# Optimization experiments

Hardware: AMD Instinct MI355X
Metric: run time of the kernel (lower is better)

The kernel has to match this reference:

```python
import jax, jax.numpy as jnp
import numpy as np
import math

B, D, L, H, K, CONV_N = 32, 128, 1024, 8, 7, 4
DK = D // H
EPS = 1e-5


def make_pos_encoding():
    i = np.arange(D, dtype=np.float64)
    freqs = np.where(i % 2 == 0, 10000.0 ** (-i / D), -(10000.0 ** ((1 - i) / D)))
    phases = np.where(i % 2 == 0, 0.0, math.pi / 2)
    pos = np.arange(L, dtype=np.float64)[None, :]  # [1, L]
    pe = np.sin(pos * freqs[:, None] + phases[:, None])  # [D, L]
    return jnp.asarray(pe, dtype=jnp.float32)


def layer_norm_2d(x, w, b):
    # nn.LayerNorm([D, L]) on [B, D, L]: normalize jointly over last two dims
    mu = jnp.mean(x, axis=(1, 2), keepdims=True)
    var = jnp.var(x, axis=(1, 2), keepdims=True)
    return (x - mu) * jax.lax.rsqrt(var + EPS) * w[None] + b[None]


def setup_inputs():
    key = jax.random.key(0)
    ks = jax.random.split(key, 24)
    s = 0.05
    x = jax.random.normal(ks[0], (B, D, L), jnp.float32)
    lengths = jax.random.randint(ks[1], (B,), L // 2, L + 1)
    mask = (jnp.arange(L)[None, :] >= lengths[:, None]).astype(jnp.float32)  # 1 = pad
    inp = {
        "x": x,
        "mask": mask,
        "pos_enc": make_pos_encoding(),
        "normb_w": jnp.ones((D, L), jnp.float32),
        "normb_b": jnp.zeros((D, L), jnp.float32),
        "dw_w": jax.random.normal(ks[2], (CONV_N, D, K), jnp.float32) * s,
        "dw_b": jnp.zeros((CONV_N, D), jnp.float32),
        "pw_w": jax.random.normal(ks[3], (CONV_N, D, D), jnp.float32) * s,
        "pw_b": jnp.zeros((CONV_N, D), jnp.float32),
        "norms_w": jnp.ones((CONV_N, D, L), jnp.float32),
        "norms_b": jnp.zeros((CONV_N, D, L), jnp.float32),
        "qw": jax.random.normal(ks[4], (D, D), jnp.float32) * s,
        "qb": jnp.zeros((D,), jnp.float32),
        "kw": jax.random.normal(ks[5], (D, D), jnp.float32) * s,
        "kb": jnp.zeros((D,), jnp.float32),
        "vw": jax.random.normal(ks[6], (D, D), jnp.float32) * s,
        "vb": jnp.zeros((D,), jnp.float32),
        "aw": jax.random.normal(ks[7], (D, D), jnp.float32) * s,  # attention output fc
        "ab": jnp.zeros((D,), jnp.float32),
        "norme_w": jnp.ones((D, L), jnp.float32),
        "norme_b": jnp.zeros((D, L), jnp.float32),
        "fw": jax.random.normal(ks[8], (D, D), jnp.float32) * s,  # final fc
        "fb": jnp.zeros((D,), jnp.float32),
    }
    return inp


def reference(x, mask, pos_enc, normb_w, normb_b, dw_w, dw_b, pw_w, pw_b,
              norms_w, norms_b, qw, qb, kw, kb, vw, vb, aw, ab,
              norme_w, norme_b, fw, fb):
    # positional encoding + pre-LN
    out = x + pos_enc[None]
    res = out
    out = layer_norm_2d(out, normb_w, normb_b)

    # conv stack (eval mode: dropout is identity)
    for i in range(CONV_N):
        h = jax.lax.conv_general_dilated(
            out, dw_w[i][:, None, :],  # depthwise: [D, 1, K]
            window_strides=(1,), padding=[(K // 2, K // 2)],
            dimension_numbers=("NCH", "OIH", "NCH"),
            feature_group_count=D) + dw_b[i][None, :, None]
        h = jnp.einsum("bcl,oc->bol", h, pw_w[i]) + pw_b[i][None, :, None]
        out = jax.nn.relu(h) + res
        res = out
        out = layer_norm_2d(out, norms_w[i], norms_b[i])

    # multi-head self-attention (manual bmm-softmax-bmm, scale 1/sqrt(d_k))
    xt = jnp.swapaxes(out, 1, 2)  # [B, L, D]
    q = (xt @ qw.T + qb).reshape(B, L, H, DK)
    k = (xt @ kw.T + kb).reshape(B, L, H, DK)
    v = (xt @ vw.T + vb).reshape(B, L, H, DK)
    scores = jnp.einsum("bqhd,bkhd->bhqk", q, k) * (1.0 / math.sqrt(DK))
    m = mask[:, None, None, :]  # broadcast over heads and query dim
    scores = scores * (1.0 - m) + m * (-1e30)
    attn = jax.nn.softmax(scores, axis=-1)
    o = jnp.einsum("bhqk,bkhd->bqhd", attn, v).reshape(B, L, D)
    o = o @ aw.T + ab
    o = jnp.swapaxes(o, 1, 2)  # [B, D, L]

    out = o + res
    res = out
    out = layer_norm_2d(out, norme_w, norme_b)
    out = jnp.einsum("bdl,ed->bel", out, fw) + fb[None, :, None]
    out = jax.nn.relu(out) + res
    return out
```

## Files before the change

### kernel.cpp

```cpp
#include <hip/hip_runtime.h>

#define NB 32
#define ND 128
#define NL 1024
#define NDL (ND*NL)
#define STATS_B 16
#define STATS_R (32*STATS_B)

typedef __attribute__((ext_vector_type(8))) short bf16x8;
typedef __attribute__((ext_vector_type(4))) float f32x4;
typedef unsigned short u16;

__device__ __forceinline__ f32x4 mfma_bf16_16x16x32(bf16x8 a, bf16x8 b, f32x4 c) {
#if defined(__HIP_DEVICE_COMPILE__)
  return __builtin_amdgcn_mfma_f32_16x16x32_bf16(a, b, c, 0, 0, 0);
#else
  return c;
#endif
}

__device__ __forceinline__ float exp2fast(float x) {
#if defined(__HIP_DEVICE_COMPILE__) && __has_builtin(__builtin_amdgcn_exp2f)
  return __builtin_amdgcn_exp2f(x);
#elif defined(__HIP_DEVICE_COMPILE__)
  return __expf(x * 0.6931471805599453f);
#else
  return x;
#endif
}

__device__ __forceinline__ float bf2f(u16 u) {
  union { unsigned u; float f; } c; c.u = ((unsigned)u) << 16; return c.f;
}
__device__ __forceinline__ u16 bf16rnd(float f) {
  union { float f; unsigned u; } c; c.f = f;
  return (u16)((c.u + 0x7FFFu + ((c.u >> 16) & 1u)) >> 16);
}
__device__ __forceinline__ unsigned packpair(float a, float b) {
  return (unsigned)bf16rnd(a) | ((unsigned)bf16rnd(b) << 16);
}
__device__ __forceinline__ unsigned packtrunc(float a, float b) {
  unsigned ua = __float_as_uint(a), ub = __float_as_uint(b);
  return (ub & 0xFFFF0000u) | (ua >> 16);
}
__device__ __forceinline__ bf16x8 packbf8(float4 a, float4 b) {
  union { unsigned u[4]; bf16x8 v; } r;
  r.u[0] = packpair(a.x, a.y); r.u[1] = packpair(a.z, a.w);
  r.u[2] = packpair(b.x, b.y); r.u[3] = packpair(b.z, b.w);
  return r.v;
}

__device__ __forceinline__ void blockRedAtomic(float s, float sq, float* base) {
  __shared__ float red[32];
#pragma unroll
  for (int off = 32; off > 0; off >>= 1) {
    s  += __shfl_down(s, off, 64);
    sq += __shfl_down(sq, off, 64);
  }
  int wave = threadIdx.x >> 6;
  int nw = blockDim.x >> 6;
  if ((threadIdx.x & 63) == 0) { red[wave*2] = s; red[wave*2+1] = sq; }
  __syncthreads();
  if (threadIdx.x == 0) {
    float ts = 0.f, tq = 0.f;
    for (int i = 0; i < nw; ++i) { ts += red[i*2]; tq += red[i*2+1]; }
    unsafeAtomicAdd(base,     ts);
    unsafeAtomicAdd(base + 1, tq);
  }
}

__global__ void k_zero(float* stats) {
  int t = threadIdx.x;
#pragma unroll
  for (int i = 0; i < 3; ++i) stats[i*1024 + t] = 0.f;
}

__global__ __launch_bounds__(256) void k_addpos(const float* __restrict__ x,
                                                const float* __restrict__ pe,
                                                u16* __restrict__ res,
                                                float* __restrict__ stats0) {
  int b = blockIdx.x >> 6;
  int off = ((blockIdx.x & 63) << 11) + (threadIdx.x << 3);
  const float4* xp = (const float4*)(x + (size_t)b*NDL + off);
  const float4* pp = (const float4*)(pe + off);
  float s = 0.f, sq = 0.f;
  float rv[8];
#pragma unroll
  for (int i = 0; i < 2; ++i) {
    float4 a = xp[i], p = pp[i];
    rv[i*4+0] = a.x + p.x; rv[i*4+1] = a.y + p.y;
    rv[i*4+2] = a.z + p.z; rv[i*4+3] = a.w + p.w;
  }
#pragma unroll
  for (int j = 0; j < 8; ++j) { s += rv[j]; sq += rv[j]*rv[j]; }
  uint4 pk;
  pk.x = packpair(rv[0], rv[1]); pk.y = packpair(rv[2], rv[3]);
  pk.z = packpair(rv[4], rv[5]); pk.w = packpair(rv[6], rv[7]);
  *(uint4*)(res + (size_t)b*NDL + off) = pk;
  blockRedAtomic(s, sq, stats0 + b*STATS_B);
}


__device__ __forceinline__ void load_w_frags16(const float* __restrict__ W,
                                               int wo, int lo, int hi, bf16x8 af[4]) {
#pragma unroll
  for (int kk = 0; kk < 4; ++kk) {
    const float4* wp = (const float4*)(W + (size_t)(wo + lo)*128 + kk*32 + hi*8);
    af[kk] = packbf8(wp[0], wp[1]);
  }
}

__device__ __forceinline__ void mfma_core16(const unsigned* xs, bf16x8 af[4],
                                            int lo, int hi, f32x4 acc[4]) {
#pragma unroll
  for (int ln = 0; ln < 4; ++ln) {
#pragma unroll
    for (int kk = 0; kk < 4; ++kk) {
      int l = ln*16 + lo;
      int off = (l*256 + kk*64 + hi*16) ^ ((lo & 7) << 4);
      bf16x8 bf = *(const bf16x8*)((const char*)xs + off);
      acc[ln] = mfma_bf16_16x16x32(af[kk], bf, acc[ln]);
    }
  }
}

__device__ __forceinline__ void conv_row8(const u16* __restrict__ srow,
                                          const float* __restrict__ lwrow,
                                          const float* __restrict__ lbrow,
                                          int base, float mu, float rstd,
                                          const float* wk, float bias0,
                                          float* h ) {
  float wa[14];
  bool interior = (base >= 4) && (base + 12 <= NL);
  if (interior) {
    const uint2* sp = (const uint2*)(srow + base - 4);
    const float4* wp = (const float4*)(lwrow + base - 4);
    const float4* bp = (const float4*)(lbrow + base - 4);
#pragma unroll
    for (int qd = 0; qd < 4; ++qd) {
      uint2 sv2 = sp[qd];
      float4 w4 = wp[qd], b4 = bp[qd];
      float sv[4] = {bf2f((u16)(sv2.x & 0xFFFF)), bf2f((u16)(sv2.x >> 16)),
                     bf2f((u16)(sv2.y & 0xFFFF)), bf2f((u16)(sv2.y >> 16))};
      float wv[4] = {w4.x, w4.y, w4.z, w4.w};
      float bv[4] = {b4.x, b4.y, b4.z, b4.w};
#pragma unroll
      for (int e = 0; e < 4; ++e) {
        int j = qd*4 + e - 1;
        if (j >= 0 && j < 14)
          wa[j] = (sv[e] - mu)*rstd*wv[e] + bv[e];
      }
    }
  } else {
#pragma unroll
    for (int j = 0; j < 14; ++j) {
      int gl = base + j - 3;
      float v = 0.f;
      if (gl >= 0 && gl < NL)
        v = (bf2f(srow[gl]) - mu)*rstd*lwrow[gl] + lbrow[gl];
      wa[j] = v;
    }
  }
#pragma unroll
  for (int l = 0; l < 8; ++l) {
    float acc = bias0;
#pragma unroll
    for (int j = 0; j < 7; ++j) acc += wa[l+j]*wk[j];
    h[l] = acc;
  }
}

template<int MODE>
__global__ __launch_bounds__(512) void k_gemm_mfma(
    const u16* __restrict__ src16, const float* __restrict__ W,
    const float* __restrict__ bias,
    const u16* __restrict__ res16, u16* __restrict__ wr16,
    float* __restrict__ outf,
    const float* __restrict__ lnw, const float* __restrict__ lnb,
    const float* __restrict__ dww, const float* __restrict__ dwb,
    const float* __restrict__ statsIn, float* __restrict__ statsOut) {
  __shared__ unsigned xs[4096];
  int b  = blockIdx.x >> 4;
  int l0 = (blockIdx.x & 15) << 6;
  int tid = threadIdx.x;
  int wave = tid >> 6, lane = tid & 63;
  int lo = lane & 15, hi = lane >> 4;
  int wo = wave * 16;

  float mu = 0.f, rstd = 0.f;
  if (MODE == 0 || MODE == 3) {
    mu = statsIn[b*STATS_B] * (1.f/NDL);
    rstd = rsqrtf(statsIn[b*STATS_B + 1]*(1.f/NDL) - mu*mu + 1e-5f);
  }

  if (MODE == 0) {
    int c2 = tid >> 3, lq = tid & 7;
    int c = c2*2, base = l0 + lq*8;
    float wk0[7], wk1[7];
#pragma unroll
    for (int j = 0; j < 7; ++j) { wk0[j] = dww[c*7 + j]; wk1[j] = dww[(c+1)*7 + j]; }
    const u16* sa = src16 + (size_t)b*NDL + (size_t)c*NL;
    const float* la  = lnw + (size_t)c*NL;
    const float* lbv = lnb + (size_t)c*NL;
    float h0[8], h1[8];
    conv_row8(sa,      la,      lbv,      base, mu, rstd, wk0, dwb[c],   h0);
    conv_row8(sa + NL, la + NL, lbv + NL, base, mu, rstd, wk1, dwb[c+1], h1);
#pragma unroll
    for (int l = 0; l < 8; ++l) {
      int ll = lq*8 + l;
      xs[(ll << 6) | (c2 ^ ((ll & 7) << 2))] = packpair(h0[l], h1[l]);
    }
  } else if (MODE == 1) {
    for (int i = tid; i < 1024; i += 512) {
      int c2 = i >> 4, lq = (i & 15) << 2;
      int c = c2*2;
      const u16* sp = src16 + (size_t)b*NDL + (size_t)c*NL + l0 + lq;
      uint2 ra = *(const uint2*)sp;
      uint2 rb = *(const uint2*)(sp + NL);
      unsigned wv[4];
      wv[0] = (ra.x & 0xFFFFu) | (rb.x << 16);
      wv[1] = (ra.x >> 16)     | (rb.x & 0xFFFF0000u);
      wv[2] = (ra.y & 0xFFFFu) | (rb.y << 16);
      wv[3] = (ra.y >> 16)     | (rb.y & 0xFFFF0000u);
#pragma unroll
      for (int j = 0; j < 4; ++j) {
        int l = lq + j;
        xs[(l << 6) | (c2 ^ ((l & 7) << 2))] = wv[j];
      }
    }
  } else {
    for (int i = tid; i < 1024; i += 512) {
      int c2 = i >> 4, lq = (i & 15) << 2;
      int c = c2*2;
      const u16* sp = src16 + (size_t)b*NDL + (size_t)c*NL + l0 + lq;
      uint2 ra = *(const uint2*)sp;
      uint2 rb = *(const uint2*)(sp + NL);
      float sa[4] = {bf2f((u16)(ra.x & 0xFFFF)), bf2f((u16)(ra.x >> 16)),
                     bf2f((u16)(ra.y & 0xFFFF)), bf2f((u16)(ra.y >> 16))};
      float sb[4] = {bf2f((u16)(rb.x & 0xFFFF)), bf2f((u16)(rb.x >> 16)),
                     bf2f((u16)(rb.y & 0xFFFF)), bf2f((u16)(rb.y >> 16))};
      size_t gi = (size_t)c*NL + l0 + lq;
      float4 w0 = *(const float4*)(lnw + gi), w1 = *(const float4*)(lnw + gi + NL);
      float4 bb0 = *(const float4*)(lnb + gi), bb1 = *(const float4*)(lnb + gi + NL);
      float va[4] = {(sa[0]-mu)*rstd*w0.x + bb0.x, (sa[1]-mu)*rstd*w0.y + bb0.y,
                     (sa[2]-mu)*rstd*w0.z + bb0.z, (sa[3]-mu)*rstd*w0.w + bb0.w};
      float vb[4] = {(sb[0]-mu)*rstd*w1.x + bb1.x, (sb[1]-mu)*rstd*w1.y + bb1.y,
                     (sb[2]-mu)*rstd*w1.z + bb1.z, (sb[3]-mu)*rstd*w1.w + bb1.w};
#pragma unroll
      for (int j = 0; j < 4; ++j) {
        int l = lq + j;
        xs[(l << 6) | (c2 ^ ((l & 7) << 2))] = packpair(va[j], vb[j]);
      }
    }
  }

  bf16x8 af[4];
  load_w_frags16(W, wo, lo, hi, af);
  f32x4 acc[4];
#pragma unroll
  for (int ln = 0; ln < 4; ++ln) acc[ln] = (f32x4){0.f,0.f,0.f,0.f};

  __syncthreads();
  mfma_core16(xs, af, lo, hi, acc);

  if (MODE == 0 || MODE == 1) {
    float s = 0.f, sq = 0.f;
#pragma unroll
    for (int ln = 0; ln < 4; ++ln) {
      int l = l0 + ln*16 + lo;
#pragma unroll
      for (int r = 0; r < 4; ++r) {
        int o = wo + hi*4 + r;
        size_t gi = ((size_t)b*ND + o)*NL + l;
        float v = acc[ln][r] + bias[o];
        if (MODE == 0) v = fmaxf(v, 0.f);
        v += bf2f(res16[gi]);
        wr16[gi] = bf16rnd(v);
        s += v; sq += v*v;
      }
    }
    blockRedAtomic(s, sq, statsOut + b*STATS_B);
  } else {
#pragma unroll
    for (int ln = 0; ln < 4; ++ln) {
      int l = l0 + ln*16 + lo;
#pragma unroll
      for (int r = 0; r < 4; ++r) {
        int o = wo + hi*4 + r;
        size_t gi = ((size_t)b*ND + o)*NL + l;
        outf[gi] = fmaxf(acc[ln][r] + bias[o], 0.f) + bf2f(res16[gi]);
      }
    }
  }
}

__global__ __launch_bounds__(512) void k_qkv_mfma(
    const u16* __restrict__ src16,
    const float* __restrict__ qw, const float* __restrict__ kw, const float* __restrict__ vw,
    const float* __restrict__ qb, const float* __restrict__ kb, const float* __restrict__ vb,
    u16* __restrict__ qo, u16* __restrict__ ko, u16* __restrict__ vo,
    const float* __restrict__ lnw, const float* __restrict__ lnb,
    const float* __restrict__ statsIn) {
  __shared__ unsigned xs[4096];
  int b  = blockIdx.x >> 4;
  int l0 = (blockIdx.x & 15) << 6;
  int tid = threadIdx.x;
  int wave = tid >> 6, lane = tid & 63;
  int lo = lane & 15, hi = lane >> 4;
  int wo = wave * 16;

  float mu = statsIn[b*STATS_B] * (1.f/NDL);
  float rstd = rsqrtf(statsIn[b*STATS_B + 1]*(1.f/NDL) - mu*mu + 1e-5f);
  for (int i = tid; i < 1024; i += 512) {
    int c2 = i >> 4, lq = (i & 15) << 2;
    int c = c2*2;
    const u16* sp = src16 + (size_t)b*NDL + (size_t)c*NL + l0 + lq;
    uint2 ra = *(const uint2*)sp;
    uint2 rb = *(const uint2*)(sp + NL);
    float sa[4] = {bf2f((u16)(ra.x & 0xFFFF)), bf2f((u16)(ra.x >> 16)),
                   bf2f((u16)(ra.y & 0xFFFF)), bf2f((u16)(ra.y >> 16))};
    float sb[4] = {bf2f((u16)(rb.x & 0xFFFF)), bf2f((u16)(rb.x >> 16)),
                   bf2f((u16)(rb.y & 0xFFFF)), bf2f((u16)(rb.y >> 16))};
    size_t gi = (size_t)c*NL + l0 + lq;
    float4 w0 = *(const float4*)(lnw + gi), w1 = *(const float4*)(lnw + gi + NL);
    float4 bb0 = *(const float4*)(lnb + gi), bb1 = *(const float4*)(lnb + gi + NL);
    float va[4] = {(sa[0]-mu)*rstd*w0.x + bb0.x, (sa[1]-mu)*rstd*w0.y + bb0.y,
                   (sa[2]-mu)*rstd*w0.z + bb0.z, (sa[3]-mu)*rstd*w0.w + bb0.w};
    float vb4[4] = {(sb[0]-mu)*rstd*w1.x + bb1.x, (sb[1]-mu)*rstd*w1.y + bb1.y,
                    (sb[2]-mu)*rstd*w1.z + bb1.z, (sb[3]-mu)*rstd*w1.w + bb1.w};
#pragma unroll
    for (int j = 0; j < 4; ++j) {
      int l = lq + j;
      xs[(l << 6) | (c2 ^ ((l & 7) << 2))] = packpair(va[j], vb4[j]);
    }
  }
  __syncthreads();

  const float* Ws[3] = {qw, kw, vw};
  const float* Bs[3] = {qb, kb, vb};
  u16* Os[3] = {qo, ko, vo};
#pragma unroll 1
  for (int mat = 0; mat < 3; ++mat) {
    bf16x8 af[4];
    load_w_frags16(Ws[mat], wo, lo, hi, af);
    f32x4 acc[4];
#pragma unroll
    for (int ln = 0; ln < 4; ++ln) acc[ln] = (f32x4){0.f,0.f,0.f,0.f};
    mfma_core16(xs, af, lo, hi, acc);
    float oscale = (mat == 0) ? 0.25f*1.4426950408889634f : 1.0f;
    const float* bias = Bs[mat];
    u16* op = Os[mat];
#pragma unroll
    for (int ln = 0; ln < 4; ++ln) {
      int l = l0 + ln*16 + lo;
      int o4 = wo + hi*4;
      float vx = (acc[ln][0] + bias[o4+0]) * oscale;
      float vy = (acc[ln][1] + bias[o4+1]) * oscale;
      float vz = (acc[ln][2] + bias[o4+2]) * oscale;
      float vw4 = (acc[ln][3] + bias[o4+3]) * oscale;
      uint2 pk; pk.x = packpair(vx, vy); pk.y = packpair(vz, vw4);
      *(uint2*)(op + ((size_t)b*NL + l)*ND + o4) = pk;
    }
  }
}

template<bool MASKED>
__device__ __forceinline__ void attn_tile(bf16x8 kf0, bf16x8 kf1, bf16x8 vf,
                                          bf16x8 onesf, const bf16x8 qf[4],
                                          f32x4 acc[4], f32x4 dacc[4],
                                          int kb, int len, int hi) {
#pragma unroll
  for (int qt = 0; qt < 4; ++qt) {
    f32x4 z = (f32x4){0.f,0.f,0.f,0.f};
    f32x4 s0 = mfma_bf16_16x16x32(kf0, qf[qt], z);
    f32x4 s1 = mfma_bf16_16x16x32(kf1, qf[qt], z);
    float e[8];
#pragma unroll
    for (int r = 0; r < 4; ++r) {
      float e0 = exp2fast(s0[r]);
      float e1 = exp2fast(s1[r]);
      if (MASKED) {
        e0 = (kb + hi*4 + r < len)      ? e0 : 0.f;
        e1 = (kb + 16 + hi*4 + r < len) ? e1 : 0.f;
      }
      e[r] = e0; e[r+4] = e1;
    }
    union { unsigned u[4]; bf16x8 v; } pu;
    pu.u[0] = packtrunc(e[0], e[1]);
    pu.u[1] = packtrunc(e[2], e[3]);
    pu.u[2] = packtrunc(e[4], e[5]);
    pu.u[3] = packtrunc(e[6], e[7]);
    acc[qt]  = mfma_bf16_16x16x32(vf,    pu.v, acc[qt]);
    dacc[qt] = mfma_bf16_16x16x32(onesf, pu.v, dacc[qt]);
  }
}

__global__ __launch_bounds__(512) void k_attn_fused(
    const u16* __restrict__ q, const u16* __restrict__ k,
    const u16* __restrict__ v, const float* __restrict__ mask,
    u16* __restrict__ att_t) {
  __shared__ short kv[32768];
  __shared__ int slen_sh;
  int bid = blockIdx.x;
  int b  = bid >> 4;
  int h  = (bid >> 1) & 7;
  int qh = bid & 1;
  int tid = threadIdx.x;
  const float* mrow = mask + (size_t)b*NL;

  if (tid == 0) slen_sh = 0;
  __syncthreads();
  {
    int cnt = 0;
    for (int i = tid; i < NL; i += 512) cnt += (mrow[i] == 0.f) ? 1 : 0;
#pragma unroll
    for (int off = 32; off > 0; off >>= 1) cnt += __shfl_down(cnt, off, 64);
    if ((tid & 63) == 0) atomicAdd(&slen_sh, cnt);
  }
  __syncthreads();
  int len = slen_sh;
  int nkt = (len + 31) >> 5;
  int kstage = nkt << 5;

  for (int idx = tid; idx < 4096; idx += 512) {
    int key = idx >> 2, dq = idx & 3;
    if (key >= kstage) break;
    int dk = dq*4;
    uint2 kd; kd.x = 0u; kd.y = 0u;
    if (key < len) kd = *(const uint2*)(k + ((size_t)b*NL + key)*ND + h*16 + dk);
    int kt = key >> 5, w = key & 31;
    int t16 = w >> 4, klo = w & 15;
    int khi = dk >> 3, ii = dk & 7;
    unsigned* dst = (unsigned*)(kv + kt*512 + t16*256 + (khi*16 + klo)*8 + ii);
    dst[0] = kd.x; dst[1] = kd.y;
  }
  for (int idx = tid; idx < 2048; idx += 512) {
    int keyp = idx >> 2, vq = idx & 3;
    int key = keyp*2;
    if (key >= kstage) break;
    int vlo = vq*4;
    uint2 ra, rb; ra.x = ra.y = rb.x = rb.y = 0u;
    size_t voff = ((size_t)b*NL + key)*ND + h*16 + vlo;
    if (key < len)     ra = *(const uint2*)(v + voff);
    if (key + 1 < len) rb = *(const uint2*)(v + voff + ND);
    unsigned wv[4];
    wv[0] = (ra.x & 0xFFFFu) | (rb.x << 16);
    wv[1] = (ra.x >> 16)     | (rb.x & 0xFFFF0000u);
    wv[2] = (ra.y & 0xFFFFu) | (rb.y << 16);
    wv[3] = (ra.y >> 16)     | (rb.y & 0xFFFF0000u);
    int kt = key >> 5, w = key & 31;
    int vhi, ii;
    if (w < 16) { vhi = w >> 2; ii = w & 3; }
    else        { vhi = (w - 16) >> 2; ii = 4 + (w & 3); }
#pragma unroll
    for (int e = 0; e < 4; ++e)
      *(unsigned*)(kv + 16384 + kt*512 + (vhi*16 + vlo + e)*8 + ii) = wv[e];
  }
  __syncthreads();

  int wave = tid >> 6, lane = tid & 63;
  int lo = lane & 15, hi = lane >> 4;
  int q0 = qh*512 + wave*64;

  bf16x8 qf[4];
#pragma unroll
  for (int qt = 0; qt < 4; ++qt) {
    if (hi < 2) {
      union { uint4 u; bf16x8 v; } qu;
      qu.u = *(const uint4*)(q + ((size_t)b*NL + q0 + qt*16 + lo)*ND + h*16 + hi*8);
      qf[qt] = qu.v;
    } else {
      qf[qt] = (bf16x8){0,0,0,0,0,0,0,0};
    }
  }
  const short oneb = (short)0x3F80;
  bf16x8 onesf = (bf16x8){oneb,oneb,oneb,oneb,oneb,oneb,oneb,oneb};
  f32x4 acc[4], dacc[4];
#pragma unroll
  for (int qt = 0; qt < 4; ++qt) {
    acc[qt]  = (f32x4){0.f,0.f,0.f,0.f};
    dacc[qt] = (f32x4){0.f,0.f,0.f,0.f};
  }

  int fullt = len >> 5;
  int l32 = hi*16 + lo;

  bf16x8 cka = (bf16x8){0,0,0,0,0,0,0,0}, ckb = cka, cv;
  if (hi < 2) {
    cka = *(const bf16x8*)(kv + l32*8);
    ckb = *(const bf16x8*)(kv + 256 + l32*8);
  }
  cv = *(const bf16x8*)(kv + 16384 + lane*8);

  for (int kt = 0; kt < nkt; ++kt) {
    bf16x8 nka = cka, nkb = ckb, nv = cv;
    if (kt + 1 < nkt) {
      if (hi < 2) {
        nka = *(const bf16x8*)(kv + (kt+1)*512 + l32*8);
        nkb = *(const bf16x8*)(kv + (kt+1)*512 + 256 + l32*8);
      }
      nv = *(const bf16x8*)(kv + 16384 + (kt+1)*512 + lane*8);
    }
    if (kt < fullt) attn_tile<false>(cka, ckb, cv, onesf, qf, acc, dacc, kt*32, len, hi);
    else            attn_tile<true >(cka, ckb, cv, onesf, qf, acc, dacc, kt*32, len, hi);
    cka = nka; ckb = nkb; cv = nv;
  }
#pragma unroll
  for (int qt = 0; qt < 4; ++qt) {
    float inv = 1.f / dacc[qt][0];
    size_t obase = ((size_t)b*ND + h*16)*NL + q0 + qt*16 + lo;
#pragma unroll
    for (int r = 0; r < 4; ++r)
      att_t[obase + (size_t)(hi*4 + r)*NL] = bf16rnd(acc[qt][r] * inv);
  }
}

extern "C" void kernel_launch(void* const* d_in, const int* in_sizes, int n_in,
                              void* d_out, int out_size, void* d_ws, size_t ws_size,
                              hipStream_t stream) {
  (void)in_sizes; (void)n_in; (void)out_size; (void)ws_size;
  const float* x       = (const float*)d_in[0];
  const float* mask    = (const float*)d_in[1];
  const float* pe      = (const float*)d_in[2];
  const float* normb_w = (const float*)d_in[3];
  const float* normb_b = (const float*)d_in[4];
  const float* dw_w    = (const float*)d_in[5];
  const float* dw_b    = (const float*)d_in[6];
  const float* pw_w    = (const float*)d_in[7];
  const float* pw_b    = (const float*)d_in[8];
  const float* norms_w = (const float*)d_in[9];
  const float* norms_b = (const float*)d_in[10];
  const float* qw      = (const float*)d_in[11];
  const float* qb      = (const float*)d_in[12];
  const float* kw      = (const float*)d_in[13];
  const float* kb      = (const float*)d_in[14];
  const float* vw      = (const float*)d_in[15];
  const float* vb      = (const float*)d_in[16];
  const float* aw      = (const float*)d_in[17];
  const float* ab      = (const float*)d_in[18];
  const float* norme_w = (const float*)d_in[19];
  const float* norme_b = (const float*)d_in[20];
  const float* fw      = (const float*)d_in[21];
  const float* fb      = (const float*)d_in[22];

  float* out = (float*)d_out;
  float* ws  = (float*)d_ws;
  const size_t NT = (size_t)NB*ND*NL;
  u16* resA = (u16*)ws;
  u16* resB = (u16*)(ws + NT/2);
  u16* qb16 = (u16*)(ws + NT);
  u16* kb16 = (u16*)(ws + 3*NT/2);
  u16* vb16 = (u16*)(ws + 2*NT);
  float* stats = ws + 3*NT;
  u16* att16 = resB;

  k_zero<<<dim3(1), dim3(1024), 0, stream>>>(stats);
  k_addpos<<<dim3(2048), dim3(256), 0, stream>>>(x, pe, resA, stats);

  for (int i = 0; i < 4; ++i) {
    const float* lw = (i == 0) ? normb_w : norms_w + (size_t)(i-1)*NDL;
    const float* lb = (i == 0) ? normb_b : norms_b + (size_t)(i-1)*NDL;
    const u16* rsrc = (i & 1) ? resB : resA;
    u16*       rdst = (i & 1) ? resA : resB;
    k_gemm_mfma<0><<<dim3(NB*16), dim3(512), 0, stream>>>(
        rsrc, pw_w + i*ND*ND, pw_b + i*ND, rsrc, rdst, nullptr,
        lw, lb, dw_w + i*ND*7, dw_b + i*ND,
        stats + i*STATS_R, stats + (i+1)*STATS_R);
  }

  const float* ln3w = norms_w + (size_t)3*NDL;
  const float* ln3b = norms_b + (size_t)3*NDL;
  k_qkv_mfma<<<dim3(NB*16), dim3(512), 0, stream>>>(
      resA, qw, kw, vw, qb, kb, vb, qb16, kb16, vb16, ln3w, ln3b, stats + 4*STATS_R);

  k_attn_fused<<<dim3(NB*8*2), dim3(512), 0, stream>>>(qb16, kb16, vb16, mask, att16);

  k_gemm_mfma<1><<<dim3(NB*16), dim3(512), 0, stream>>>(
      att16, aw, ab, resA, resA, nullptr, nullptr, nullptr, nullptr, nullptr,
      nullptr, stats + 5*STATS_R);
  k_gemm_mfma<3><<<dim3(NB*16), dim3(512), 0, stream>>>(
      resA, fw, fb, resA, nullptr, out, norme_w, norme_b, nullptr, nullptr,
      stats + 5*STATS_R, nullptr);
}
```

Before: 173.0 us.

## Precompute sequence lengths, load K directly from global, prefetch residuals in GEMM

Adds a small kernel that computes per-batch valid lengths once, so the attention kernel no longer scans the mask in every block. The attention kernel drops K staging into LDS and instead loads K fragments straight from global memory in the loop, which halves LDS use and may raise occupancy but makes the inner loop depend on global-memory latency. The GEMM kernel also issues its residual loads before the MFMA core so their latency overlaps with compute. The lenbuf is placed after the stats region in the workspace.

```diff
diff --git a/kernel.cpp b/kernel.cpp
--- a/kernel.cpp
+++ b/kernel.cpp
@@ -73,6 +73,21 @@
   int t = threadIdx.x;
 #pragma unroll
   for (int i = 0; i < 3; ++i) stats[i*1024 + t] = 0.f;
+}
+
+__global__ __launch_bounds__(256) void k_len(const float* __restrict__ mask,
+                                             int* __restrict__ lenbuf) {
+  __shared__ int csh;
+  int b = blockIdx.x, tid = threadIdx.x;
+  if (tid == 0) csh = 0;
+  __syncthreads();
+  int cnt = 0;
+  for (int i = tid; i < NL; i += 256) cnt += (mask[(size_t)b*NL + i] == 0.f) ? 1 : 0;
+#pragma unroll
+  for (int off = 32; off > 0; off >>= 1) cnt += __shfl_down(cnt, off, 64);
+  if ((tid & 63) == 0) atomicAdd(&csh, cnt);
+  __syncthreads();
+  if (tid == 0) lenbuf[b] = csh;
 }
 
 __global__ __launch_bounds__(256) void k_addpos(const float* __restrict__ x,
@@ -254,6 +269,13 @@
     }
   }
 
+  u16 rpre[16];
+#pragma unroll
+  for (int ln = 0; ln < 4; ++ln)
+#pragma unroll
+    for (int r = 0; r < 4; ++r)
+      rpre[ln*4+r] = res16[((size_t)b*ND + wo + hi*4 + r)*NL + l0 + ln*16 + lo];
+
   bf16x8 af[4];
   load_w_frags16(W, wo, lo, hi, af);
   f32x4 acc[4];
@@ -274,7 +296,7 @@
         size_t gi = ((size_t)b*ND + o)*NL + l;
         float v = acc[ln][r] + bias[o];
         if (MODE == 0) v = fmaxf(v, 0.f);
-        v += bf2f(res16[gi]);
+        v += bf2f(rpre[ln*4+r]);
         wr16[gi] = bf16rnd(v);
         s += v; sq += v*v;
       }
@@ -288,7 +310,7 @@
       for (int r = 0; r < 4; ++r) {
         int o = wo + hi*4 + r;
         size_t gi = ((size_t)b*ND + o)*NL + l;
-        outf[gi] = fmaxf(acc[ln][r] + bias[o], 0.f) + bf2f(res16[gi]);
+        outf[gi] = fmaxf(acc[ln][r] + bias[o], 0.f) + bf2f(rpre[ln*4+r]);
       }
     }
   }
@@ -395,45 +417,26 @@
   }
 }
 
+__device__ __forceinline__ bf16x8 ldKrow(const u16* kbase, int key, int hi) {
+  union { uint4 u; bf16x8 v; } r;
+  r.u = *(const uint4*)(kbase + (size_t)key*ND + hi*8);
+  return r.v;
+}
+
 __global__ __launch_bounds__(512) void k_attn_fused(
     const u16* __restrict__ q, const u16* __restrict__ k,
-    const u16* __restrict__ v, const float* __restrict__ mask,
+    const u16* __restrict__ v, const int* __restrict__ lenbuf,
     u16* __restrict__ att_t) {
-  __shared__ short kv[32768];
-  __shared__ int slen_sh;
+  __shared__ short kv[16384];
   int bid = blockIdx.x;
   int b  = bid >> 4;
   int h  = (bid >> 1) & 7;
   int qh = bid & 1;
   int tid = threadIdx.x;
-  const float* mrow = mask + (size_t)b*NL;
-
-  if (tid == 0) slen_sh = 0;
-  __syncthreads();
-  {
-    int cnt = 0;
-    for (int i = tid; i < NL; i += 512) cnt += (mrow[i] == 0.f) ? 1 : 0;
-#pragma unroll
-    for (int off = 32; off > 0; off >>= 1) cnt += __shfl_down(cnt, off, 64);
-    if ((tid & 63) == 0) atomicAdd(&slen_sh, cnt);
-  }
-  __syncthreads();
-  int len = slen_sh;
+  int len = lenbuf[b];
   int nkt = (len + 31) >> 5;
   int kstage = nkt << 5;
 
-  for (int idx = tid; idx < 4096; idx += 512) {
-    int key = idx >> 2, dq = idx & 3;
-    if (key >= kstage) break;
-    int dk = dq*4;
-    uint2 kd; kd.x = 0u; kd.y = 0u;
-    if (key < len) kd = *(const uint2*)(k + ((size_t)b*NL + key)*ND + h*16 + dk);
-    int kt = key >> 5, w = key & 31;
-    int t16 = w >> 4, klo = w & 15;
-    int khi = dk >> 3, ii = dk & 7;
-    unsigned* dst = (unsigned*)(kv + kt*512 + t16*256 + (khi*16 + klo)*8 + ii);
-    dst[0] = kd.x; dst[1] = kd.y;
-  }
   for (int idx = tid; idx < 2048; idx += 512) {
     int keyp = idx >> 2, vq = idx & 3;
     int key = keyp*2;
@@ -454,7 +457,7 @@
     else        { vhi = (w - 16) >> 2; ii = 4 + (w & 3); }
 #pragma unroll
     for (int e = 0; e < 4; ++e)
-      *(unsigned*)(kv + 16384 + kt*512 + (vhi*16 + vlo + e)*8 + ii) = wv[e];
+      *(unsigned*)(kv + kt*512 + (vhi*16 + vlo + e)*8 + ii) = wv[e];
   }
   __syncthreads();
 
@@ -483,23 +486,24 @@
   }
 
   int fullt = len >> 5;
-  int l32 = hi*16 + lo;
+  const u16* kbase = k + (size_t)b*NL*ND + h*16;
 
   bf16x8 cka = (bf16x8){0,0,0,0,0,0,0,0}, ckb = cka, cv;
   if (hi < 2) {
-    cka = *(const bf16x8*)(kv + l32*8);
-    ckb = *(const bf16x8*)(kv + 256 + l32*8);
-  }
-  cv = *(const bf16x8*)(kv + 16384 + lane*8);
+    cka = ldKrow(kbase, lo, hi);
+    ckb = ldKrow(kbase, 16 + lo, hi);
+  }
+  cv = *(const bf16x8*)(kv + lane*8);
 
   for (int kt = 0; kt < nkt; ++kt) {
     bf16x8 nka = cka, nkb = ckb, nv = cv;
     if (kt + 1 < nkt) {
+      int kb2 = (kt+1)*32;
       if (hi < 2) {
-        nka = *(const bf16x8*)(kv + (kt+1)*512 + l32*8);
-        nkb = *(const bf16x8*)(kv + (kt+1)*512 + 256 + l32*8);
-      }
-      nv = *(const bf16x8*)(kv + 16384 + (kt+1)*512 + lane*8);
+        nka = ldKrow(kbase, kb2 + lo, hi);
+        nkb = ldKrow(kbase, kb2 + 16 + lo, hi);
+      }
+      nv = *(const bf16x8*)(kv + (kt+1)*512 + lane*8);
     }
     if (kt < fullt) attn_tile<false>(cka, ckb, cv, onesf, qf, acc, dacc, kt*32, len, hi);
     else            attn_tile<true >(cka, ckb, cv, onesf, qf, acc, dacc, kt*32, len, hi);
@@ -552,9 +556,11 @@
   u16* kb16 = (u16*)(ws + 3*NT/2);
   u16* vb16 = (u16*)(ws + 2*NT);
   float* stats = ws + 3*NT;
+  int* lenbuf = (int*)(stats + 6*STATS_R);
   u16* att16 = resB;
 
   k_zero<<<dim3(1), dim3(1024), 0, stream>>>(stats);
+  k_len<<<dim3(NB), dim3(256), 0, stream>>>(mask, lenbuf);
   k_addpos<<<dim3(2048), dim3(256), 0, stream>>>(x, pe, resA, stats);
 
   for (int i = 0; i < 4; ++i) {
@@ -573,7 +579,7 @@
   k_qkv_mfma<<<dim3(NB*16), dim3(512), 0, stream>>>(
       resA, qw, kw, vw, qb, kb, vb, qb16, kb16, vb16, ln3w, ln3b, stats + 4*STATS_R);
 
-  k_attn_fused<<<dim3(NB*8*2), dim3(512), 0, stream>>>(qb16, kb16, vb16, mask, att16);
+  k_attn_fused<<<dim3(NB*8*2), dim3(512), 0, stream>>>(qb16, kb16, vb16, lenbuf, att16);
 
   k_gemm_mfma<1><<<dim3(NB*16), dim3(512), 0, stream>>>(
       att16, aw, ab, resA, resA, nullptr, nullptr, nullptr, nullptr, nullptr,
```

Measured after the change: 172.1 us. No clear change (-0.5%).
